# Performance work log

Measured on AMD Instinct MI355X. Metric: run time of the kernel, lower is better.

Reference implementation:

```python
import jax, jax.numpy as jnp
import numpy as np

B, S, HID = 2, 2048, 2048
N_HEADS = 16
HEAD_DIM = HID // N_HEADS  # 128
ROPE_THETA = 10000.0
MAX_SEQ = 4096


def _rope_cache(position_ids, head_dim, theta=ROPE_THETA, max_seq=MAX_SEQ):
    # standard RoPE cache: cos/sin of shape [B, S, head_dim//2]
    half = head_dim // 2
    inv_freq = 1.0 / theta ** (jnp.arange(half, dtype=jnp.float32) / half)
    t = jnp.arange(max_seq, dtype=jnp.float32)
    freqs = jnp.outer(t, inv_freq)                      # [max_seq, half]
    pos = jnp.clip(position_ids, 0, max_seq - 1)
    return jnp.cos(freqs)[pos], jnp.sin(freqs)[pos]     # [B, S, half]


def _apply_rope(q, k, cos, sin):
    # q,k: [B, H, S, D]; cos/sin: [B, S, D/2] -> [B, 1, S, D/2]
    cos = cos[:, None, :, :]
    sin = sin[:, None, :, :]
    q1, q2 = jnp.split(q, 2, axis=-1)
    k1, k2 = jnp.split(k, 2, axis=-1)
    q_rot = jnp.concatenate([q1 * cos - q2 * sin, q2 * cos + q1 * sin], axis=-1)
    k_rot = jnp.concatenate([k1 * cos - k2 * sin, k2 * cos + k1 * sin], axis=-1)
    return q_rot, k_rot


def setup_inputs() -> dict:
    key = jax.random.key(0)
    ks = jax.random.split(key, 6)
    hidden_states = jax.random.normal(ks[0], (B, S, HID), dtype=jnp.float32)
    # additive causal mask, broadcastable over batch and heads
    causal = jnp.tril(jnp.ones((S, S), dtype=bool))
    attention_mask = jnp.where(causal, 0.0, -1e9).astype(jnp.float32)[None, None]
    position_ids = jnp.broadcast_to(jnp.arange(S, dtype=jnp.int32)[None, :], (B, S))
    scale = 0.02
    Wq = jax.random.normal(ks[1], (HID, N_HEADS * HEAD_DIM), dtype=jnp.float32) * scale
    Wk = jax.random.normal(ks[2], (HID, N_HEADS * HEAD_DIM), dtype=jnp.float32) * scale
    Wv = jax.random.normal(ks[3], (HID, N_HEADS * HEAD_DIM), dtype=jnp.float32) * scale
    Wo = jax.random.normal(ks[4], (N_HEADS * HEAD_DIM, HID), dtype=jnp.float32) * scale
    zeros = jnp.zeros((HID,), dtype=jnp.float32)
    return {
        "hidden_states": hidden_states,
        "attention_mask": attention_mask,
        "position_ids": position_ids,
        "Wq": Wq, "bq": zeros,
        "Wk": Wk, "bk": zeros,
        "Wv": Wv, "bv": zeros,
        "Wo": Wo, "bo": zeros,
    }


def reference(hidden_states, attention_mask, position_ids,
              Wq, bq, Wk, bk, Wv, bv, Wo, bo):
    b, s, _ = hidden_states.shape
    q = (hidden_states @ Wq + bq).reshape(b, s, N_HEADS, HEAD_DIM).transpose(0, 2, 1, 3)
    k = (hidden_states @ Wk + bk).reshape(b, s, N_HEADS, HEAD_DIM).transpose(0, 2, 1, 3)
    v = (hidden_states @ Wv + bv).reshape(b, s, N_HEADS, HEAD_DIM).transpose(0, 2, 1, 3)

    cos, sin = _rope_cache(position_ids, HEAD_DIM)
    q, k = _apply_rope(q, k, cos, sin)

    scores = jnp.einsum("bhqd,bhkd->bhqk", q, k) / jnp.sqrt(jnp.float32(HEAD_DIM))
    scores = scores + attention_mask
    weights = jax.nn.softmax(scores, axis=-1)
    attn = jnp.einsum("bhqk,bhkd->bhqd", weights, v)  # [B,H,S,D]
    attn = attn.transpose(0, 2, 1, 3).reshape(b, s, N_HEADS * HEAD_DIM)
    return attn @ Wo + bo
```

## Files before the change

### kernel.cpp

```cpp
#include <hip/hip_runtime.h>
#include <hip/hip_bf16.h>

typedef __bf16 bf16;
typedef bf16 bf16x4 __attribute__((ext_vector_type(4)));
typedef bf16 bf16x8 __attribute__((ext_vector_type(8)));
typedef float f32x4 __attribute__((ext_vector_type(4)));

#define B_ 2
#define S_ 2048
#define HID_ 2048
#define NH_ 16
#define HD_ 128
#define M_TOT (B_ * S_)
#define RSCALE 0.08838834764831845f
#define LN10000_OVER_64 0.14391156f

#define OFF_XB   0ull
#define OFF_WQT  (OFF_XB  + (size_t)M_TOT*HID_*2)
#define OFF_WKT  (OFF_WQT + (size_t)HID_*HID_*2)
#define OFF_WVT  (OFF_WKT + (size_t)HID_*HID_*2)
#define OFF_WOT  (OFF_WVT + (size_t)HID_*HID_*2)
#define OFF_QB   (OFF_WOT + (size_t)HID_*HID_*2)
#define OFF_KB   (OFF_QB  + (size_t)M_TOT*HID_*2)
#define OFF_VTB  (OFF_KB  + (size_t)M_TOT*HID_*2)
#define OFF_AB   (OFF_VTB + (size_t)M_TOT*HID_*2)

__device__ __forceinline__ void gload16(const bf16* g, bf16* l) {
    typedef const __attribute__((address_space(1))) unsigned int gu32;
    typedef __attribute__((address_space(3))) unsigned int lu32;
    __builtin_amdgcn_global_load_lds((gu32*)g, (lu32*)l, 16, 0, 0);
}

__global__ __launch_bounds__(256) void cvt_x(const float* __restrict__ x,
                                             bf16* __restrict__ o) {
    size_t i = ((size_t)blockIdx.x * 256 + threadIdx.x) * 4;
    float4 v = *(const float4*)(x + i);
    bf16x4 r; r[0] = (bf16)v.x; r[1] = (bf16)v.y; r[2] = (bf16)v.z; r[3] = (bf16)v.w;
    *(bf16x4*)(o + i) = r;
}

__global__ __launch_bounds__(256) void trans_w(const float* w0, const float* w1,
                                               const float* w2, const float* w3,
                                               bf16* o0, bf16* o1, bf16* o2, bf16* o3) {
    const float* W; bf16* O;
    switch (blockIdx.z) {
        case 0: W = w0; O = o0; break;
        case 1: W = w1; O = o1; break;
        case 2: W = w2; O = o2; break;
        default: W = w3; O = o3; break;
    }
    __shared__ float t[64][65];
    int tid = threadIdx.x;
    int nt0 = blockIdx.x * 64, kt0 = blockIdx.y * 64;
    #pragma unroll
    for (int p = 0; p < 4; ++p) {
        int r = p * 16 + (tid >> 4);
        int c = (tid & 15) * 4;
        float4 v = *(const float4*)(W + (size_t)(kt0 + r) * HID_ + nt0 + c);
        t[r][c + 0] = v.x; t[r][c + 1] = v.y; t[r][c + 2] = v.z; t[r][c + 3] = v.w;
    }
    __syncthreads();
    #pragma unroll
    for (int p = 0; p < 4; ++p) {
        int rr = p * 16 + (tid >> 4);
        int cc = (tid & 15) * 4;
        bf16x4 v;
        v[0] = (bf16)t[cc + 0][rr]; v[1] = (bf16)t[cc + 1][rr];
        v[2] = (bf16)t[cc + 2][rr]; v[3] = (bf16)t[cc + 3][rr];
        *(bf16x4*)(O + (size_t)(nt0 + rr) * HID_ + kt0 + cc) = v;
    }
}

template <int MODE>
__global__ __launch_bounds__(256) void gemm_k(const bf16* __restrict__ A,
                                              const bf16* __restrict__ Bt,
                                              const float* __restrict__ bias,
                                              const int* __restrict__ pos_ids,
                                              void* __restrict__ out) {
    __shared__ bf16 Al[128][64];
    __shared__ bf16 Bl[128][64];
    const int tid = threadIdx.x;
    const int l = tid & 63, w = tid >> 6;
    const int ln = l & 15, lg = l >> 4;
    const int bm = blockIdx.y, bn = blockIdx.x;

    f32x4 acc[2][8] = {};

    for (int k0 = 0; k0 < HID_; k0 += 64) {
        __syncthreads();
        #pragma unroll
        for (int j = 0; j < 4; ++j) {
            int r0 = w * 32 + j * 8;
            int r = r0 + (l >> 3);
            int c = (l & 7) * 8;
            gload16(A  + (size_t)(bm * 128 + r) * HID_ + k0 + c, &Al[r0][0]);
            gload16(Bt + (size_t)(bn * 128 + r) * HID_ + k0 + c, &Bl[r0][0]);
        }
        __syncthreads();
        #pragma unroll
        for (int kk = 0; kk < 2; ++kk) {
            bf16x8 af[2], bfv[8];
            #pragma unroll
            for (int fm = 0; fm < 2; ++fm)
                af[fm] = *(const bf16x8*)&Al[w * 32 + fm * 16 + ln][kk * 32 + lg * 8];
            #pragma unroll
            for (int fn = 0; fn < 8; ++fn)
                bfv[fn] = *(const bf16x8*)&Bl[fn * 16 + ln][kk * 32 + lg * 8];
            #pragma unroll
            for (int fm = 0; fm < 2; ++fm)
                #pragma unroll
                for (int fn = 0; fn < 8; ++fn)
                    acc[fm][fn] = __builtin_amdgcn_mfma_f32_16x16x32_bf16(
                        af[fm], bfv[fn], acc[fm][fn], 0, 0, 0);
        }
    }

    #pragma unroll
    for (int fm = 0; fm < 2; ++fm) {
        #pragma unroll
        for (int i = 0; i < 4; ++i) {
            int m_g = bm * 128 + w * 32 + fm * 16 + lg * 4 + i;
            if (MODE == 3) {
                float* O = (float*)out;
                #pragma unroll
                for (int fn = 0; fn < 8; ++fn) {
                    int n_g = bn * 128 + fn * 16 + ln;
                    O[(size_t)m_g * HID_ + n_g] = acc[fm][fn][i] + bias[n_g];
                }
            } else if (MODE == 2) {
                int b = m_g >> 11, s = m_g & (S_ - 1);
                bf16* O = (bf16*)out;
                #pragma unroll
                for (int fn = 0; fn < 8; ++fn) {
                    int d = fn * 16 + ln;
                    float v = acc[fm][fn][i] + bias[bn * 128 + d];
                    O[((size_t)(b * NH_ + bn) * HD_ + d) * S_ + s] = (bf16)v;
                }
            } else {
                int b = m_g >> 11, s = m_g & (S_ - 1);
                int pos = pos_ids[m_g];
                pos = pos < 0 ? 0 : (pos > 4095 ? 4095 : pos);
                size_t base = ((size_t)(b * NH_ + bn) * S_ + s) * HD_;
                bf16* O = (bf16*)out;
                #pragma unroll
                for (int fn = 0; fn < 4; ++fn) {
                    int j = fn * 16 + ln;
                    float x1 = acc[fm][fn][i]     + bias[bn * 128 + j];
                    float x2 = acc[fm][fn + 4][i] + bias[bn * 128 + j + 64];
                    float invf = __expf(-(float)j * LN10000_OVER_64);
                    float ang = (float)pos * invf;
                    float sn, cs;
                    __sincosf(ang, &sn, &cs);
                    float y1 = x1 * cs - x2 * sn;
                    float y2 = x2 * cs + x1 * sn;
                    if (MODE == 0) { y1 *= RSCALE; y2 *= RSCALE; }
                    O[base + j]      = (bf16)y1;
                    O[base + j + 64] = (bf16)y2;
                }
            }
        }
    }
}

__global__ __launch_bounds__(512) void attn_k(const bf16* __restrict__ Q,
                                              const bf16* __restrict__ K,
                                              const bf16* __restrict__ Vt,
                                              bf16* __restrict__ O) {
    __shared__ bf16 Kl[64][136];
    __shared__ bf16 Vl[128][72];
    __shared__ bf16 Pl[8][16][72];
    const int tid = threadIdx.x;
    const int l = tid & 63, w = tid >> 6;
    const int ln = l & 15, lg = l >> 4;
    const int pair = blockIdx.x, bh = blockIdx.y;

    const bf16* Qb = Q  + (size_t)bh * S_ * HD_;
    const bf16* Kb = K  + (size_t)bh * S_ * HD_;
    const bf16* Vb = Vt + (size_t)bh * S_ * HD_;
    const int b = bh >> 4, h = bh & (NH_ - 1);

    uint4 kr[2], vr[2];

    for (int rep = 0; rep < 2; ++rep) {
        const int j = rep ? (15 - pair) : pair;
        const int nkt = 2 * j + 2;
        const int qrow = j * 128 + w * 16 + ln;
        const int qg0  = j * 128 + w * 16 + lg * 4;

        bf16x8 qf[4];
        #pragma unroll
        for (int kk = 0; kk < 4; ++kk)
            qf[kk] = *(const bf16x8*)(Qb + (size_t)qrow * HD_ + kk * 32 + lg * 8);

        float m_run[4], l_run[4];
        #pragma unroll
        for (int i = 0; i < 4; ++i) { m_run[i] = -1e30f; l_run[i] = 0.f; }
        f32x4 oacc[8] = {};

        #pragma unroll
        for (int m = 0; m < 2; ++m) {
            int f = m * 512 + tid;
            kr[m] = *(const uint4*)(Kb + (size_t)(f >> 4) * HD_ + (f & 15) * 8);
            vr[m] = *(const uint4*)(Vb + (size_t)(f >> 3) * S_ + (f & 7) * 8);
        }

        for (int kt = 0; kt < nkt; ++kt) {
            __syncthreads();
            #pragma unroll
            for (int m = 0; m < 2; ++m) {
                int f = m * 512 + tid;
                *(uint4*)&Kl[f >> 4][(f & 15) * 8] = kr[m];
                *(uint4*)&Vl[f >> 3][(f & 7) * 8] = vr[m];
            }
            __syncthreads();
            if (kt + 1 < nkt) {
                #pragma unroll
                for (int m = 0; m < 2; ++m) {
                    int f = m * 512 + tid;
                    kr[m] = *(const uint4*)(Kb + (size_t)((kt + 1) * 64 + (f >> 4)) * HD_ + (f & 15) * 8);
                    vr[m] = *(const uint4*)(Vb + (size_t)(f >> 3) * S_ + (kt + 1) * 64 + (f & 7) * 8);
                }
            }

            f32x4 sacc[4] = {};
            #pragma unroll
            for (int kk = 0; kk < 4; ++kk) {
                bf16x8 kf[4];
                #pragma unroll
                for (int n = 0; n < 4; ++n)
                    kf[n] = *(const bf16x8*)&Kl[n * 16 + ln][kk * 32 + lg * 8];
                #pragma unroll
                for (int n = 0; n < 4; ++n)
                    sacc[n] = __builtin_amdgcn_mfma_f32_16x16x32_bf16(qf[kk], kf[n], sacc[n], 0, 0, 0);
            }

            if (kt >= 2 * j) {
                #pragma unroll
                for (int n = 0; n < 4; ++n)
                    #pragma unroll
                    for (int i = 0; i < 4; ++i) {
                        int kg = kt * 64 + n * 16 + ln;
                        if (kg > qg0 + i) sacc[n][i] = -1e30f;
                    }
            }

            float mt[4];
            #pragma unroll
            for (int i = 0; i < 4; ++i) {
                mt[i] = fmaxf(fmaxf(sacc[0][i], sacc[1][i]), fmaxf(sacc[2][i], sacc[3][i]));
                #pragma unroll
                for (int d = 1; d < 16; d <<= 1)
                    mt[i] = fmaxf(mt[i], __shfl_xor(mt[i], d));
            }
            float scale[4], rs[4];
            #pragma unroll
            for (int i = 0; i < 4; ++i) {
                float mnew = fmaxf(m_run[i], mt[i]);
                scale[i] = __expf(m_run[i] - mnew);
                m_run[i] = mnew;
                rs[i] = 0.f;
            }
            #pragma unroll
            for (int n = 0; n < 4; ++n)
                #pragma unroll
                for (int i = 0; i < 4; ++i) {
                    float p = __expf(sacc[n][i] - m_run[i]);
                    sacc[n][i] = p;
                    rs[i] += p;
                }
            #pragma unroll
            for (int i = 0; i < 4; ++i) {
                #pragma unroll
                for (int d = 1; d < 16; d <<= 1)
                    rs[i] += __shfl_xor(rs[i], d);
                l_run[i] = l_run[i] * scale[i] + rs[i];
            }
            #pragma unroll
            for (int dn = 0; dn < 8; ++dn)
                #pragma unroll
                for (int i = 0; i < 4; ++i)
                    oacc[dn][i] *= scale[i];

            #pragma unroll
            for (int n = 0; n < 4; ++n)
                #pragma unroll
                for (int i = 0; i < 4; ++i)
                    Pl[w][lg * 4 + i][n * 16 + ln] = (bf16)sacc[n][i];

            #pragma unroll
            for (int kk = 0; kk < 2; ++kk) {
                bf16x8 pf = *(const bf16x8*)&Pl[w][ln][kk * 32 + lg * 8];
                #pragma unroll
                for (int dn = 0; dn < 8; ++dn) {
                    bf16x8 vf = *(const bf16x8*)&Vl[dn * 16 + ln][kk * 32 + lg * 8];
                    oacc[dn] = __builtin_amdgcn_mfma_f32_16x16x32_bf16(pf, vf, oacc[dn], 0, 0, 0);
                }
            }
        }

        #pragma unroll
        for (int i = 0; i < 4; ++i) {
            float inv = 1.0f / l_run[i];
            int s = j * 128 + w * 16 + lg * 4 + i;
            #pragma unroll
            for (int dn = 0; dn < 8; ++dn) {
                int d = dn * 16 + ln;
                O[((size_t)(b * S_ + s)) * HID_ + h * HD_ + d] = (bf16)(oacc[dn][i] * inv);
            }
        }
    }
}

extern "C" void kernel_launch(void* const* d_in, const int* in_sizes, int n_in,
                              void* d_out, int out_size, void* d_ws, size_t ws_size,
                              hipStream_t stream) {
    const float* X    = (const float*)d_in[0];
    const int*   pos  = (const int*)d_in[2];
    const float* Wq   = (const float*)d_in[3];
    const float* bq   = (const float*)d_in[4];
    const float* Wk   = (const float*)d_in[5];
    const float* bk   = (const float*)d_in[6];
    const float* Wv   = (const float*)d_in[7];
    const float* bv   = (const float*)d_in[8];
    const float* Wo   = (const float*)d_in[9];
    const float* bo   = (const float*)d_in[10];
    float* Out = (float*)d_out;

    char* ws = (char*)d_ws;
    bf16* Xb  = (bf16*)(ws + OFF_XB);
    bf16* Wqt = (bf16*)(ws + OFF_WQT);
    bf16* Wkt = (bf16*)(ws + OFF_WKT);
    bf16* Wvt = (bf16*)(ws + OFF_WVT);
    bf16* Wot = (bf16*)(ws + OFF_WOT);
    bf16* Qb  = (bf16*)(ws + OFF_QB);
    bf16* Kb  = (bf16*)(ws + OFF_KB);
    bf16* Vtb = (bf16*)(ws + OFF_VTB);
    bf16* Ab  = (bf16*)(ws + OFF_AB);

    cvt_x<<<(M_TOT * HID_) / (256 * 4), 256, 0, stream>>>(X, Xb);
    trans_w<<<dim3(32, 32, 4), 256, 0, stream>>>(Wq, Wk, Wv, Wo, Wqt, Wkt, Wvt, Wot);

    dim3 gg(HID_ / 128, M_TOT / 128);
    gemm_k<0><<<gg, 256, 0, stream>>>(Xb, Wqt, bq, pos, (void*)Qb);
    gemm_k<1><<<gg, 256, 0, stream>>>(Xb, Wkt, bk, pos, (void*)Kb);
    gemm_k<2><<<gg, 256, 0, stream>>>(Xb, Wvt, bv, pos, (void*)Vtb);

    attn_k<<<dim3(8, B_ * NH_), 512, 0, stream>>>(Qb, Kb, Vtb, Ab);

    gemm_k<3><<<gg, 256, 0, stream>>>(Ab, Wot, bo, pos, (void*)Out);
}
```

Baseline: 367.4 us.

## Process both paired query tiles in one K/V sweep in attention kernel

```diff
diff --git a/kernel.cpp b/kernel.cpp
--- a/kernel.cpp
+++ b/kernel.cpp
@@ -168,86 +168,95 @@
                                               bf16* __restrict__ O) {
     __shared__ bf16 Kl[64][136];
     __shared__ bf16 Vl[128][72];
-    __shared__ bf16 Pl[8][16][72];
+    __shared__ bf16 Pl[8][2][16][72];
     const int tid = threadIdx.x;
     const int l = tid & 63, w = tid >> 6;
     const int ln = l & 15, lg = l >> 4;
-    const int pair = blockIdx.x, bh = blockIdx.y;
+    const int jlo = blockIdx.x, bh = blockIdx.y;
+    const int jhi = 15 - jlo;
+    const int nkt = 2 * jhi + 2;
 
     const bf16* Qb = Q  + (size_t)bh * S_ * HD_;
     const bf16* Kb = K  + (size_t)bh * S_ * HD_;
     const bf16* Vb = Vt + (size_t)bh * S_ * HD_;
     const int b = bh >> 4, h = bh & (NH_ - 1);
 
+    bf16x8 qf[2][4];
+    #pragma unroll
+    for (int t = 0; t < 2; ++t) {
+        int qrow = (t ? jhi : jlo) * 128 + w * 16 + ln;
+        #pragma unroll
+        for (int kk = 0; kk < 4; ++kk)
+            qf[t][kk] = *(const bf16x8*)(Qb + (size_t)qrow * HD_ + kk * 32 + lg * 8);
+    }
+    const int qg0[2] = { jlo * 128 + w * 16 + lg * 4, jhi * 128 + w * 16 + lg * 4 };
+
+    float m_run[2][4], l_run[2][4];
+    #pragma unroll
+    for (int t = 0; t < 2; ++t)
+        #pragma unroll
+        for (int i = 0; i < 4; ++i) { m_run[t][i] = -1e30f; l_run[t][i] = 0.f; }
+    f32x4 oacc[2][8] = {};
+
     uint4 kr[2], vr[2];
-
-    for (int rep = 0; rep < 2; ++rep) {
-        const int j = rep ? (15 - pair) : pair;
-        const int nkt = 2 * j + 2;
-        const int qrow = j * 128 + w * 16 + ln;
-        const int qg0  = j * 128 + w * 16 + lg * 4;
-
-        bf16x8 qf[4];
-        #pragma unroll
-        for (int kk = 0; kk < 4; ++kk)
-            qf[kk] = *(const bf16x8*)(Qb + (size_t)qrow * HD_ + kk * 32 + lg * 8);
-
-        float m_run[4], l_run[4];
-        #pragma unroll
-        for (int i = 0; i < 4; ++i) { m_run[i] = -1e30f; l_run[i] = 0.f; }
-        f32x4 oacc[8] = {};
-
+    #pragma unroll
+    for (int m = 0; m < 2; ++m) {
+        int f = m * 512 + tid;
+        kr[m] = *(const uint4*)(Kb + (size_t)(f >> 4) * HD_ + (f & 15) * 8);
+        vr[m] = *(const uint4*)(Vb + (size_t)(f >> 3) * S_ + (f & 7) * 8);
+    }
+
+    for (int kt = 0; kt < nkt; ++kt) {
+        const bool lo_act = (kt < 2 * jlo + 2);
+        __syncthreads();
         #pragma unroll
         for (int m = 0; m < 2; ++m) {
             int f = m * 512 + tid;
-            kr[m] = *(const uint4*)(Kb + (size_t)(f >> 4) * HD_ + (f & 15) * 8);
-            vr[m] = *(const uint4*)(Vb + (size_t)(f >> 3) * S_ + (f & 7) * 8);
-        }
-
-        for (int kt = 0; kt < nkt; ++kt) {
-            __syncthreads();
+            *(uint4*)&Kl[f >> 4][(f & 15) * 8] = kr[m];
+            *(uint4*)&Vl[f >> 3][(f & 7) * 8] = vr[m];
+        }
+        __syncthreads();
+        if (kt + 1 < nkt) {
             #pragma unroll
             for (int m = 0; m < 2; ++m) {
                 int f = m * 512 + tid;
-                *(uint4*)&Kl[f >> 4][(f & 15) * 8] = kr[m];
-                *(uint4*)&Vl[f >> 3][(f & 7) * 8] = vr[m];
-            }
-            __syncthreads();
-            if (kt + 1 < nkt) {
-                #pragma unroll
-                for (int m = 0; m < 2; ++m) {
-                    int f = m * 512 + tid;
-                    kr[m] = *(const uint4*)(Kb + (size_t)((kt + 1) * 64 + (f >> 4)) * HD_ + (f & 15) * 8);
-                    vr[m] = *(const uint4*)(Vb + (size_t)(f >> 3) * S_ + (kt + 1) * 64 + (f & 7) * 8);
-                }
-            }
-
-            f32x4 sacc[4] = {};
-            #pragma unroll
-            for (int kk = 0; kk < 4; ++kk) {
-                bf16x8 kf[4];
-                #pragma unroll
-                for (int n = 0; n < 4; ++n)
-                    kf[n] = *(const bf16x8*)&Kl[n * 16 + ln][kk * 32 + lg * 8];
-                #pragma unroll
-                for (int n = 0; n < 4; ++n)
-                    sacc[n] = __builtin_amdgcn_mfma_f32_16x16x32_bf16(qf[kk], kf[n], sacc[n], 0, 0, 0);
-            }
-
-            if (kt >= 2 * j) {
+                kr[m] = *(const uint4*)(Kb + (size_t)((kt + 1) * 64 + (f >> 4)) * HD_ + (f & 15) * 8);
+                vr[m] = *(const uint4*)(Vb + (size_t)(f >> 3) * S_ + (kt + 1) * 64 + (f & 7) * 8);
+            }
+        }
+
+        f32x4 sacc[2][4] = {};
+        #pragma unroll
+        for (int kk = 0; kk < 4; ++kk) {
+            bf16x8 kfr[4];
+            #pragma unroll
+            for (int n = 0; n < 4; ++n)
+                kfr[n] = *(const bf16x8*)&Kl[n * 16 + ln][kk * 32 + lg * 8];
+            #pragma unroll
+            for (int n = 0; n < 4; ++n) {
+                sacc[1][n] = __builtin_amdgcn_mfma_f32_16x16x32_bf16(qf[1][kk], kfr[n], sacc[1][n], 0, 0, 0);
+                if (lo_act)
+                    sacc[0][n] = __builtin_amdgcn_mfma_f32_16x16x32_bf16(qf[0][kk], kfr[n], sacc[0][n], 0, 0, 0);
+            }
+        }
+
+        #pragma unroll
+        for (int t = 0; t < 2; ++t) {
+            if (t == 0 && !lo_act) continue;
+            const int jt = t ? jhi : jlo;
+            if (kt >= 2 * jt) {
                 #pragma unroll
                 for (int n = 0; n < 4; ++n)
                     #pragma unroll
                     for (int i = 0; i < 4; ++i) {
                         int kg = kt * 64 + n * 16 + ln;
-                        if (kg > qg0 + i) sacc[n][i] = -1e30f;
+                        if (kg > qg0[t] + i) sacc[t][n][i] = -1e30f;
                     }
             }
-
             float mt[4];
             #pragma unroll
             for (int i = 0; i < 4; ++i) {
-                mt[i] = fmaxf(fmaxf(sacc[0][i], sacc[1][i]), fmaxf(sacc[2][i], sacc[3][i]));
+                mt[i] = fmaxf(fmaxf(sacc[t][0][i], sacc[t][1][i]), fmaxf(sacc[t][2][i], sacc[t][3][i]));
                 #pragma unroll
                 for (int d = 1; d < 16; d <<= 1)
                     mt[i] = fmaxf(mt[i], __shfl_xor(mt[i], d));
@@ -255,17 +264,17 @@
             float scale[4], rs[4];
             #pragma unroll
             for (int i = 0; i < 4; ++i) {
-                float mnew = fmaxf(m_run[i], mt[i]);
-                scale[i] = __expf(m_run[i] - mnew);
-                m_run[i] = mnew;
+                float mnew = fmaxf(m_run[t][i], mt[i]);
+                scale[i] = __expf(m_run[t][i] - mnew);
+                m_run[t][i] = mnew;
                 rs[i] = 0.f;
             }
             #pragma unroll
             for (int n = 0; n < 4; ++n)
                 #pragma unroll
                 for (int i = 0; i < 4; ++i) {
-                    float p = __expf(sacc[n][i] - m_run[i]);
-                    sacc[n][i] = p;
+                    float p = __expf(sacc[t][n][i] - m_run[t][i]);
+                    sacc[t][n][i] = p;
                     rs[i] += p;
                 }
             #pragma unroll
@@ -273,39 +282,48 @@
                 #pragma unroll
                 for (int d = 1; d < 16; d <<= 1)
                     rs[i] += __shfl_xor(rs[i], d);
-                l_run[i] = l_run[i] * scale[i] + rs[i];
+                l_run[t][i] = l_run[t][i] * scale[i] + rs[i];
             }
             #pragma unroll
             for (int dn = 0; dn < 8; ++dn)
                 #pragma unroll
                 for (int i = 0; i < 4; ++i)
-                    oacc[dn][i] *= scale[i];
-
+                    oacc[t][dn][i] *= scale[i];
             #pragma unroll
             for (int n = 0; n < 4; ++n)
                 #pragma unroll
                 for (int i = 0; i < 4; ++i)
-                    Pl[w][lg * 4 + i][n * 16 + ln] = (bf16)sacc[n][i];
-
-            #pragma unroll
-            for (int kk = 0; kk < 2; ++kk) {
-                bf16x8 pf = *(const bf16x8*)&Pl[w][ln][kk * 32 + lg * 8];
-                #pragma unroll
-                for (int dn = 0; dn < 8; ++dn) {
-                    bf16x8 vf = *(const bf16x8*)&Vl[dn * 16 + ln][kk * 32 + lg * 8];
-                    oacc[dn] = __builtin_amdgcn_mfma_f32_16x16x32_bf16(pf, vf, oacc[dn], 0, 0, 0);
-                }
-            }
-        }
-
+                    Pl[w][t][lg * 4 + i][n * 16 + ln] = (bf16)sacc[t][n][i];
+        }
+
+        #pragma unroll
+        for (int kk = 0; kk < 2; ++kk) {
+            bf16x8 vfr[8];
+            #pragma unroll
+            for (int dn = 0; dn < 8; ++dn)
+                vfr[dn] = *(const bf16x8*)&Vl[dn * 16 + ln][kk * 32 + lg * 8];
+            #pragma unroll
+            for (int t = 0; t < 2; ++t) {
+                if (t == 0 && !lo_act) continue;
+                bf16x8 pf = *(const bf16x8*)&Pl[w][t][ln][kk * 32 + lg * 8];
+                #pragma unroll
+                for (int dn = 0; dn < 8; ++dn)
+                    oacc[t][dn] = __builtin_amdgcn_mfma_f32_16x16x32_bf16(pf, vfr[dn], oacc[t][dn], 0, 0, 0);
+            }
+        }
+    }
+
+    #pragma unroll
+    for (int t = 0; t < 2; ++t) {
+        const int jt = t ? jhi : jlo;
         #pragma unroll
         for (int i = 0; i < 4; ++i) {
-            float inv = 1.0f / l_run[i];
-            int s = j * 128 + w * 16 + lg * 4 + i;
+            float inv = 1.0f / l_run[t][i];
+            int s = jt * 128 + w * 16 + lg * 4 + i;
             #pragma unroll
             for (int dn = 0; dn < 8; ++dn) {
                 int d = dn * 16 + ln;
-                O[((size_t)(b * S_ + s)) * HID_ + h * HD_ + d] = (bf16)(oacc[dn][i] * inv);
+                O[((size_t)(b * S_ + s)) * HID_ + h * HD_ + d] = (bf16)(oacc[t][dn][i] * inv);
             }
         }
     }
```

After: 366.1 us. No clear change (-0.4%).

## Merge Q/K/V projections into one launch and shrink attention query tiles

Applied to the files above, without the earlier changes.

```diff
diff --git a/kernel.cpp b/kernel.cpp
--- a/kernel.cpp
+++ b/kernel.cpp
@@ -71,12 +71,97 @@
     }
 }
 
-template <int MODE>
-__global__ __launch_bounds__(256) void gemm_k(const bf16* __restrict__ A,
+__global__ __launch_bounds__(256) void gemm_qkv(const bf16* __restrict__ A,
+                                                const bf16* __restrict__ Wt3,
+                                                const float* __restrict__ bq,
+                                                const float* __restrict__ bk,
+                                                const float* __restrict__ bv,
+                                                const int* __restrict__ pos_ids,
+                                                bf16* __restrict__ out3) {
+    __shared__ bf16 Al[128][64];
+    __shared__ bf16 Bl[128][64];
+    const int tid = threadIdx.x;
+    const int l = tid & 63, w = tid >> 6;
+    const int ln = l & 15, lg = l >> 4;
+    const int bm = blockIdx.y;
+    const int sel = blockIdx.x >> 4, bnn = blockIdx.x & 15;
+    const bf16* Bt = Wt3 + (size_t)sel * HID_ * HID_ + (size_t)bnn * 128 * HID_;
+    const float* bias = sel == 0 ? bq : (sel == 1 ? bk : bv);
+
+    f32x4 acc[2][8] = {};
+
+    for (int k0 = 0; k0 < HID_; k0 += 64) {
+        __syncthreads();
+        #pragma unroll
+        for (int j = 0; j < 4; ++j) {
+            int r0 = w * 32 + j * 8;
+            int r = r0 + (l >> 3);
+            int c = (l & 7) * 8;
+            gload16(A  + (size_t)(bm * 128 + r) * HID_ + k0 + c, &Al[r0][0]);
+            gload16(Bt + (size_t)r * HID_ + k0 + c, &Bl[r0][0]);
+        }
+        __syncthreads();
+        #pragma unroll
+        for (int kk = 0; kk < 2; ++kk) {
+            bf16x8 af[2], bfv[8];
+            #pragma unroll
+            for (int fm = 0; fm < 2; ++fm)
+                af[fm] = *(const bf16x8*)&Al[w * 32 + fm * 16 + ln][kk * 32 + lg * 8];
+            #pragma unroll
+            for (int fn = 0; fn < 8; ++fn)
+                bfv[fn] = *(const bf16x8*)&Bl[fn * 16 + ln][kk * 32 + lg * 8];
+            #pragma unroll
+            for (int fm = 0; fm < 2; ++fm)
+                #pragma unroll
+                for (int fn = 0; fn < 8; ++fn)
+                    acc[fm][fn] = __builtin_amdgcn_mfma_f32_16x16x32_bf16(
+                        af[fm], bfv[fn], acc[fm][fn], 0, 0, 0);
+        }
+    }
+
+    #pragma unroll
+    for (int fm = 0; fm < 2; ++fm) {
+        #pragma unroll
+        for (int i = 0; i < 4; ++i) {
+            int m_g = bm * 128 + w * 32 + fm * 16 + lg * 4 + i;
+            int b = m_g >> 11, s = m_g & (S_ - 1);
+            if (sel == 2) {
+                bf16* O = out3 + 2 * (size_t)M_TOT * HID_;
+                #pragma unroll
+                for (int fn = 0; fn < 8; ++fn) {
+                    int d = fn * 16 + ln;
+                    float v = acc[fm][fn][i] + bias[bnn * 128 + d];
+                    O[((size_t)(b * NH_ + bnn) * HD_ + d) * S_ + s] = (bf16)v;
+                }
+            } else {
+                int pos = pos_ids[m_g];
+                pos = pos < 0 ? 0 : (pos > 4095 ? 4095 : pos);
+                size_t base = ((size_t)(b * NH_ + bnn) * S_ + s) * HD_;
+                bf16* O = out3 + (size_t)sel * M_TOT * HID_;
+                #pragma unroll
+                for (int fn = 0; fn < 4; ++fn) {
+                    int j = fn * 16 + ln;
+                    float x1 = acc[fm][fn][i]     + bias[bnn * 128 + j];
+                    float x2 = acc[fm][fn + 4][i] + bias[bnn * 128 + j + 64];
+                    float invf = __expf(-(float)j * LN10000_OVER_64);
+                    float ang = (float)pos * invf;
+                    float sn, cs;
+                    __sincosf(ang, &sn, &cs);
+                    float y1 = x1 * cs - x2 * sn;
+                    float y2 = x2 * cs + x1 * sn;
+                    if (sel == 0) { y1 *= RSCALE; y2 *= RSCALE; }
+                    O[base + j]      = (bf16)y1;
+                    O[base + j + 64] = (bf16)y2;
+                }
+            }
+        }
+    }
+}
+
+__global__ __launch_bounds__(256) void gemm_o(const bf16* __restrict__ A,
                                               const bf16* __restrict__ Bt,
                                               const float* __restrict__ bias,
-                                              const int* __restrict__ pos_ids,
-                                              void* __restrict__ out) {
+                                              float* __restrict__ out) {
     __shared__ bf16 Al[128][64];
     __shared__ bf16 Bl[128][64];
     const int tid = threadIdx.x;
@@ -116,76 +201,42 @@
     }
 
     #pragma unroll
-    for (int fm = 0; fm < 2; ++fm) {
+    for (int fm = 0; fm < 2; ++fm)
         #pragma unroll
         for (int i = 0; i < 4; ++i) {
             int m_g = bm * 128 + w * 32 + fm * 16 + lg * 4 + i;
-            if (MODE == 3) {
-                float* O = (float*)out;
-                #pragma unroll
-                for (int fn = 0; fn < 8; ++fn) {
-                    int n_g = bn * 128 + fn * 16 + ln;
-                    O[(size_t)m_g * HID_ + n_g] = acc[fm][fn][i] + bias[n_g];
-                }
-            } else if (MODE == 2) {
-                int b = m_g >> 11, s = m_g & (S_ - 1);
-                bf16* O = (bf16*)out;
-                #pragma unroll
-                for (int fn = 0; fn < 8; ++fn) {
-                    int d = fn * 16 + ln;
-                    float v = acc[fm][fn][i] + bias[bn * 128 + d];
-                    O[((size_t)(b * NH_ + bn) * HD_ + d) * S_ + s] = (bf16)v;
-                }
-            } else {
-                int b = m_g >> 11, s = m_g & (S_ - 1);
-                int pos = pos_ids[m_g];
-                pos = pos < 0 ? 0 : (pos > 4095 ? 4095 : pos);
-                size_t base = ((size_t)(b * NH_ + bn) * S_ + s) * HD_;
-                bf16* O = (bf16*)out;
-                #pragma unroll
-                for (int fn = 0; fn < 4; ++fn) {
-                    int j = fn * 16 + ln;
-                    float x1 = acc[fm][fn][i]     + bias[bn * 128 + j];
-                    float x2 = acc[fm][fn + 4][i] + bias[bn * 128 + j + 64];
-                    float invf = __expf(-(float)j * LN10000_OVER_64);
-                    float ang = (float)pos * invf;
-                    float sn, cs;
-                    __sincosf(ang, &sn, &cs);
-                    float y1 = x1 * cs - x2 * sn;
-                    float y2 = x2 * cs + x1 * sn;
-                    if (MODE == 0) { y1 *= RSCALE; y2 *= RSCALE; }
-                    O[base + j]      = (bf16)y1;
-                    O[base + j + 64] = (bf16)y2;
-                }
-            }
-        }
-    }
-}
-
-__global__ __launch_bounds__(512) void attn_k(const bf16* __restrict__ Q,
+            #pragma unroll
+            for (int fn = 0; fn < 8; ++fn) {
+                int n_g = bn * 128 + fn * 16 + ln;
+                out[(size_t)m_g * HID_ + n_g] = acc[fm][fn][i] + bias[n_g];
+            }
+        }
+}
+
+__global__ __launch_bounds__(256) void attn_k(const bf16* __restrict__ Q,
                                               const bf16* __restrict__ K,
                                               const bf16* __restrict__ Vt,
                                               bf16* __restrict__ O) {
     __shared__ bf16 Kl[64][136];
     __shared__ bf16 Vl[128][72];
-    __shared__ bf16 Pl[8][16][72];
+    __shared__ bf16 Pl[4][16][72];
     const int tid = threadIdx.x;
     const int l = tid & 63, w = tid >> 6;
     const int ln = l & 15, lg = l >> 4;
-    const int pair = blockIdx.x, bh = blockIdx.y;
+    const int jp = blockIdx.x, bh = blockIdx.y;
 
     const bf16* Qb = Q  + (size_t)bh * S_ * HD_;
     const bf16* Kb = K  + (size_t)bh * S_ * HD_;
     const bf16* Vb = Vt + (size_t)bh * S_ * HD_;
     const int b = bh >> 4, h = bh & (NH_ - 1);
 
-    uint4 kr[2], vr[2];
+    uint4 kr[4], vr[4];
 
     for (int rep = 0; rep < 2; ++rep) {
-        const int j = rep ? (15 - pair) : pair;
-        const int nkt = 2 * j + 2;
-        const int qrow = j * 128 + w * 16 + ln;
-        const int qg0  = j * 128 + w * 16 + lg * 4;
+        const int j = rep ? (31 - jp) : jp;
+        const int nkt = j + 1;
+        const int qrow = j * 64 + w * 16 + ln;
+        const int qg0  = j * 64 + w * 16 + lg * 4;
 
         bf16x8 qf[4];
         #pragma unroll
@@ -198,8 +249,8 @@
         f32x4 oacc[8] = {};
 
         #pragma unroll
-        for (int m = 0; m < 2; ++m) {
-            int f = m * 512 + tid;
+        for (int m = 0; m < 4; ++m) {
+            int f = m * 256 + tid;
             kr[m] = *(const uint4*)(Kb + (size_t)(f >> 4) * HD_ + (f & 15) * 8);
             vr[m] = *(const uint4*)(Vb + (size_t)(f >> 3) * S_ + (f & 7) * 8);
         }
@@ -207,16 +258,16 @@
         for (int kt = 0; kt < nkt; ++kt) {
             __syncthreads();
             #pragma unroll
-            for (int m = 0; m < 2; ++m) {
-                int f = m * 512 + tid;
+            for (int m = 0; m < 4; ++m) {
+                int f = m * 256 + tid;
                 *(uint4*)&Kl[f >> 4][(f & 15) * 8] = kr[m];
                 *(uint4*)&Vl[f >> 3][(f & 7) * 8] = vr[m];
             }
             __syncthreads();
             if (kt + 1 < nkt) {
                 #pragma unroll
-                for (int m = 0; m < 2; ++m) {
-                    int f = m * 512 + tid;
+                for (int m = 0; m < 4; ++m) {
+                    int f = m * 256 + tid;
                     kr[m] = *(const uint4*)(Kb + (size_t)((kt + 1) * 64 + (f >> 4)) * HD_ + (f & 15) * 8);
                     vr[m] = *(const uint4*)(Vb + (size_t)(f >> 3) * S_ + (kt + 1) * 64 + (f & 7) * 8);
                 }
@@ -234,7 +285,7 @@
                     sacc[n] = __builtin_amdgcn_mfma_f32_16x16x32_bf16(qf[kk], kf[n], sacc[n], 0, 0, 0);
             }
 
-            if (kt >= 2 * j) {
+            if (kt == j) {
                 #pragma unroll
                 for (int n = 0; n < 4; ++n)
                     #pragma unroll
@@ -301,7 +352,7 @@
         #pragma unroll
         for (int i = 0; i < 4; ++i) {
             float inv = 1.0f / l_run[i];
-            int s = j * 128 + w * 16 + lg * 4 + i;
+            int s = j * 64 + w * 16 + lg * 4 + i;
             #pragma unroll
             for (int dn = 0; dn < 8; ++dn) {
                 int d = dn * 16 + ln;
@@ -340,12 +391,9 @@
     cvt_x<<<(M_TOT * HID_) / (256 * 4), 256, 0, stream>>>(X, Xb);
     trans_w<<<dim3(32, 32, 4), 256, 0, stream>>>(Wq, Wk, Wv, Wo, Wqt, Wkt, Wvt, Wot);
 
-    dim3 gg(HID_ / 128, M_TOT / 128);
-    gemm_k<0><<<gg, 256, 0, stream>>>(Xb, Wqt, bq, pos, (void*)Qb);
-    gemm_k<1><<<gg, 256, 0, stream>>>(Xb, Wkt, bk, pos, (void*)Kb);
-    gemm_k<2><<<gg, 256, 0, stream>>>(Xb, Wvt, bv, pos, (void*)Vtb);
-
-    attn_k<<<dim3(8, B_ * NH_), 512, 0, stream>>>(Qb, Kb, Vtb, Ab);
-
-    gemm_k<3><<<gg, 256, 0, stream>>>(Ab, Wot, bo, pos, (void*)Out);
-}
+    gemm_qkv<<<dim3(48, M_TOT / 128), 256, 0, stream>>>(Xb, Wqt, bq, bk, bv, pos, Qb);
+
+    attn_k<<<dim3(16, B_ * NH_), 256, 0, stream>>>(Qb, Kb, Vtb, Ab);
+
+    gemm_o<<<dim3(HID_ / 128, M_TOT / 128), 256, 0, stream>>>(Ab, Wot, bo, Out);
+}
```

New measurement: 447.0 us. +21.6%, slower.
